# Performance work log

Measured on AMD Instinct MI355X. Metric: run time of the kernel, lower is better.

## Reference

```python
import jax, jax.numpy as jnp
import numpy as np

N_NODES = 50000


def gcn_conv(x, edge_index, edge_weight, W, b):
    """PyG GCNConv: x' = D^{-1/2}(A+I)D^{-1/2} (x W) + b, with edge weights."""
    n = x.shape[0]
    x = x @ W  # transform first (PyG order): [N, d_out]
    row, col = edge_index[0], edge_index[1]  # source -> target
    # add self loops with weight 1
    loop = jnp.arange(n)
    row = jnp.concatenate([row, loop])
    col = jnp.concatenate([col, loop])
    ew = jnp.concatenate([edge_weight, jnp.ones((n,), dtype=x.dtype)])
    # symmetric normalization based on (weighted) in-degree at targets
    deg = jax.ops.segment_sum(ew, col, num_segments=n)
    dis = jnp.where(deg > 0, jax.lax.rsqrt(deg), 0.0)
    norm = dis[row] * ew * dis[col]  # [E+N]
    # gather-scale-scatter aggregation
    msg = x[row] * norm[:, None]  # [E+N, d_out]
    out = jax.ops.segment_sum(msg, col, num_segments=n)
    return out + b


def setup_inputs() -> dict:
    key = jax.random.key(0)
    ks = jax.random.split(key, 9)
    E = 800000
    bert_output = jax.random.normal(ks[0], (N_NODES, 1024), dtype=jnp.float32)
    edge_index = jax.random.randint(ks[1], (2, E), 0, N_NODES, dtype=jnp.int64)
    edge_weight = jax.random.uniform(ks[2], (E,), dtype=jnp.float32)
    s1 = 1.0 / np.sqrt(1024)
    s2 = 1.0 / np.sqrt(512)
    s3 = 1.0 / np.sqrt(128)
    W1 = jax.random.uniform(ks[3], (1024, 512), jnp.float32, -s1, s1)
    b1 = jnp.zeros((512,), jnp.float32)
    W2 = jax.random.uniform(ks[4], (512, 128), jnp.float32, -s2, s2)
    b2 = jnp.zeros((128,), jnp.float32)
    Wfc = jax.random.uniform(ks[5], (128, 14), jnp.float32, -s3, s3)
    bfc = jax.random.uniform(ks[6], (14,), jnp.float32, -s3, s3)
    return {
        "bert_output": bert_output,
        "edge_index": edge_index,
        "edge_weight": edge_weight,
        "W1": W1, "b1": b1, "W2": W2, "b2": b2, "Wfc": Wfc, "bfc": bfc,
    }


def reference(bert_output, edge_index, edge_weight, W1, b1, W2, b2, Wfc, bfc):
    h = jax.nn.relu(gcn_conv(bert_output, edge_index, edge_weight, W1, b1))
    h = jax.nn.relu(gcn_conv(h, edge_index, edge_weight, W2, b2))
    logits = h @ Wfc + bfc
    return jax.nn.sigmoid(logits)
```

## Files before the change

kernel.cpp:

```cpp
#include <hip/hip_runtime.h>
#include <stdint.h>

__device__ __forceinline__ float bf2f(unsigned short h) {
  union { uint32_t u; float f; } v; v.u = ((uint32_t)h) << 16; return v.f;
}
__device__ __forceinline__ unsigned short f2bf(float f) {
  union { float f; uint32_t u; } v; v.f = f;
  uint32_t u = v.u;
  u += 0x7FFFu + ((u >> 16) & 1u);
  return (unsigned short)(u >> 16);
}
__device__ __forceinline__ uint32_t pack2bf(float a, float b) {
  return (uint32_t)f2bf(a) | ((uint32_t)f2bf(b) << 16);
}

typedef __attribute__((ext_vector_type(8))) short short8;
typedef __attribute__((ext_vector_type(4))) float floatx4;

__global__ void bgcn_probe(const uint32_t* __restrict__ xw,
                           const uint32_t* __restrict__ iw,
                           int* __restrict__ flags) {
  if (threadIdx.x == 0 && blockIdx.x == 0) {
    int hits = 0;
    for (int i = 0; i < 256; ++i) {
      uint32_t b = (xw[i] >> 8) & 0x7F;
      if (b >= 0x38 && b <= 0x41) hits++;
    }
    flags[0] = (hits < 128) ? 1 : 0;
    int nz = 0;
    for (int i = 1; i < 128; i += 2) nz += (iw[i] != 0);
    flags[1] = (nz == 0) ? 1 : 0;
  }
}

__global__ void bgcn_cvt_f(const void* __restrict__ src, unsigned short* __restrict__ dst,
                           int n, const int* __restrict__ flags) {
  int i = blockIdx.x * 256 + threadIdx.x;
  if (i >= n) return;
  if (flags[0]) dst[i] = f2bf(((const float*)src)[i]);
  else          dst[i] = ((const unsigned short*)src)[i];
}
__global__ void bgcn_cvt_i(const void* __restrict__ src, int* __restrict__ dst,
                           int n, const int* __restrict__ flags) {
  int i = blockIdx.x * 256 + threadIdx.x;
  if (i >= n) return;
  if (flags[1]) dst[i] = (int)((const long long*)src)[i];
  else          dst[i] = ((const int*)src)[i];
}
__global__ void bgcn_cvt_t(const void* __restrict__ src, unsigned short* __restrict__ dst,
                           int kbits, int N, int total, const int* __restrict__ flags) {
  int i = blockIdx.x * 256 + threadIdx.x;
  if (i >= total) return;
  int K = 1 << kbits;
  int n = i >> kbits;
  int k = i & (K - 1);
  size_t s = (size_t)k * N + n;
  if (flags[0]) dst[i] = f2bf(((const float*)src)[s]);
  else          dst[i] = ((const unsigned short*)src)[s];
}

__global__ void bgcn_init_deg(float* __restrict__ deg, int n) {
  int i = blockIdx.x * 256 + threadIdx.x;
  if (i < n) deg[i] = 1.0f;
}
__global__ void bgcn_deg(const int* __restrict__ col, const unsigned short* __restrict__ ew,
                         float* __restrict__ deg, int E) {
  int e = blockIdx.x * 256 + threadIdx.x;
  if (e < E) atomicAdd(&deg[col[e]], bf2f(ew[e]));
}
__global__ void bgcn_dis(const float* __restrict__ deg, float* __restrict__ dis, int n) {
  int i = blockIdx.x * 256 + threadIdx.x;
  if (i < n) dis[i] = rsqrtf(deg[i]);
}

__global__ void bgcn_hist(const int* __restrict__ col, int* __restrict__ counts, int E) {
  int e = blockIdx.x * 256 + threadIdx.x;
  if (e < E) atomicAdd(&counts[col[e]], 1);
}
__global__ void bgcn_scan_block(const int* __restrict__ counts, int* __restrict__ rowptr,
                                int* __restrict__ blocksum, int n) {
  __shared__ int buf[1024];
  int gid = blockIdx.x * 1024 + threadIdx.x;
  int v = (gid < n) ? counts[gid] : 0;
  buf[threadIdx.x] = v;
  __syncthreads();
  for (int off = 1; off < 1024; off <<= 1) {
    int x = (threadIdx.x >= off) ? buf[threadIdx.x - off] : 0;
    __syncthreads();
    buf[threadIdx.x] += x;
    __syncthreads();
  }
  if (gid < n) rowptr[gid + 1] = buf[threadIdx.x];
  if (threadIdx.x == 1023) blocksum[blockIdx.x] = buf[1023];
}
__global__ void bgcn_scan_tops(int* __restrict__ blocksum, int nb) {
  if (threadIdx.x == 0 && blockIdx.x == 0) {
    int acc = 0;
    for (int i = 0; i < nb; ++i) { int v = blocksum[i]; blocksum[i] = acc; acc += v; }
  }
}
__global__ void bgcn_scan_add(int* __restrict__ rowptr, const int* __restrict__ blocksum, int n) {
  int gid = blockIdx.x * 1024 + threadIdx.x;
  if (gid < n) rowptr[gid + 1] += blocksum[blockIdx.x];
  if (gid == 0) rowptr[0] = 0;
}
__global__ void bgcn_scatter(const int* __restrict__ row, const int* __restrict__ col,
                             const unsigned short* __restrict__ ew,
                             const float* __restrict__ dis,
                             const int* __restrict__ rowptr, int* __restrict__ fill,
                             int* __restrict__ esrc, float* __restrict__ enorm, int E) {
  int e = blockIdx.x * 256 + threadIdx.x;
  if (e >= E) return;
  int r = row[e], c = col[e];
  int pos = rowptr[c] + atomicAdd(&fill[c], 1);
  esrc[pos]  = r;
  enorm[pos] = dis[r] * bf2f(ew[e]) * dis[c];
}

#define GST 40
__global__ __launch_bounds__(256, 2) void bgcn_gemm128(
    const void* __restrict__ Araw, int a_probe, const int* __restrict__ flags,
    const unsigned short* __restrict__ Bt,
    unsigned short* __restrict__ C,
    int M, int N, int K, int nblk_bits) {
  __shared__ unsigned short Abuf[128 * GST];
  __shared__ unsigned short Bbuf[128 * GST];
  const bool a_fp32 = a_probe && flags[0];
  int t = threadIdx.x;
  int wave = t >> 6, lane = t & 63;
  int bx = blockIdx.x;
  int nblk = bx & ((1 << nblk_bits) - 1);
  int mblk = bx >> nblk_bits;
  int m0 = mblk * 128, n0 = nblk * 128;

  floatx4 acc[4][4];
  #pragma unroll
  for (int i = 0; i < 4; ++i)
    #pragma unroll
    for (int j = 0; j < 4; ++j)
      #pragma unroll
      for (int r = 0; r < 4; ++r) acc[i][j][r] = 0.0f;

  int srow  = t >> 1;
  int skoff = (t & 1) * 16;
  int am = m0 + srow; if (am >= M) am = M - 1;
  const float*          Af = (const float*)Araw          + (size_t)am * K + skoff;
  const unsigned short* Ah = (const unsigned short*)Araw + (size_t)am * K + skoff;
  const unsigned short* Bp = Bt + (size_t)(n0 + srow) * K + skoff;
  unsigned short* AL = Abuf + srow * GST + skoff;
  unsigned short* BL = Bbuf + srow * GST + skoff;

  int fr = lane & 15;
  int fk = (lane >> 4) * 8;
  int mw = (wave & 1) * 64;
  int nw = (wave >> 1) * 64;

  for (int k0 = 0; k0 < K; k0 += 32) {
    uint4 a0, a1;
    if (a_fp32) {
      float4 f0 = *(const float4*)(Af + k0);
      float4 f1 = *(const float4*)(Af + k0 + 4);
      float4 f2 = *(const float4*)(Af + k0 + 8);
      float4 f3 = *(const float4*)(Af + k0 + 12);
      a0 = make_uint4(pack2bf(f0.x, f0.y), pack2bf(f0.z, f0.w),
                      pack2bf(f1.x, f1.y), pack2bf(f1.z, f1.w));
      a1 = make_uint4(pack2bf(f2.x, f2.y), pack2bf(f2.z, f2.w),
                      pack2bf(f3.x, f3.y), pack2bf(f3.z, f3.w));
    } else {
      a0 = *(const uint4*)(Ah + k0);
      a1 = *(const uint4*)(Ah + k0 + 8);
    }
    uint4 b0 = *(const uint4*)(Bp + k0);
    uint4 b1 = *(const uint4*)(Bp + k0 + 8);
    *(uint4*)AL       = a0;
    *(uint4*)(AL + 8) = a1;
    *(uint4*)BL       = b0;
    *(uint4*)(BL + 8) = b1;
    __syncthreads();

    short8 afr[4], bfr[4];
    #pragma unroll
    for (int i = 0; i < 4; ++i)
      afr[i] = *(const short8*)(Abuf + (mw + i * 16 + fr) * GST + fk);
    #pragma unroll
    for (int i = 0; i < 4; ++i)
      bfr[i] = *(const short8*)(Bbuf + (nw + i * 16 + fr) * GST + fk);
    #pragma unroll
    for (int mt = 0; mt < 4; ++mt)
      #pragma unroll
      for (int nt = 0; nt < 4; ++nt)
        acc[mt][nt] = __builtin_amdgcn_mfma_f32_16x16x32_bf16(afr[mt], bfr[nt], acc[mt][nt], 0, 0, 0);
    __syncthreads();
  }

  int col_l = lane & 15;
  int row_b = (lane >> 4) * 4;
  #pragma unroll
  for (int mt = 0; mt < 4; ++mt)
    #pragma unroll
    for (int nt = 0; nt < 4; ++nt)
      #pragma unroll
      for (int r = 0; r < 4; ++r) {
        int m = m0 + mw + mt * 16 + row_b + r;
        if (m < M)
          C[(size_t)m * N + n0 + nw + nt * 16 + col_l] = f2bf(acc[mt][nt][r]);
      }
}

template <int VPL>
__device__ __forceinline__ void loadbf(const unsigned short* p, float* out) {
  if constexpr (VPL == 8) {
    uint4 v = *(const uint4*)p;
    uint32_t w0 = v.x, w1 = v.y, w2 = v.z, w3 = v.w;
    out[0] = bf2f((unsigned short)(w0 & 0xffff)); out[1] = bf2f((unsigned short)(w0 >> 16));
    out[2] = bf2f((unsigned short)(w1 & 0xffff)); out[3] = bf2f((unsigned short)(w1 >> 16));
    out[4] = bf2f((unsigned short)(w2 & 0xffff)); out[5] = bf2f((unsigned short)(w2 >> 16));
    out[6] = bf2f((unsigned short)(w3 & 0xffff)); out[7] = bf2f((unsigned short)(w3 >> 16));
  } else {
    uint32_t v = *(const uint32_t*)p;
    out[0] = bf2f((unsigned short)(v & 0xffff)); out[1] = bf2f((unsigned short)(v >> 16));
  }
}

template <int F>
__global__ __launch_bounds__(256) void bgcn_aggregate(
    const unsigned short* __restrict__ H,
    const int* __restrict__ rowptr,
    const int* __restrict__ esrc,
    const float* __restrict__ enorm,
    const float* __restrict__ dis,
    const unsigned short* __restrict__ bias,
    unsigned short* __restrict__ Out,
    int n_nodes) {
  constexpr int VPL = F / 64;
  int lane = threadIdx.x & 63;
  int c = blockIdx.x * 4 + (threadIdx.x >> 6);
  if (c >= n_nodes) return;
  float acc[VPL];
  #pragma unroll
  for (int j = 0; j < VPL; ++j) acc[j] = 0.0f;

  int beg = rowptr[c], end = rowptr[c + 1];
  int e = beg;
  for (; e + 4 <= end; e += 4) {
    int s0 = esrc[e], s1 = esrc[e + 1], s2 = esrc[e + 2], s3 = esrc[e + 3];
    float w0 = enorm[e], w1 = enorm[e + 1], w2 = enorm[e + 2], w3 = enorm[e + 3];
    float v0[VPL], v1[VPL], v2[VPL], v3[VPL];
    loadbf<VPL>(H + (size_t)s0 * F + lane * VPL, v0);
    loadbf<VPL>(H + (size_t)s1 * F + lane * VPL, v1);
    loadbf<VPL>(H + (size_t)s2 * F + lane * VPL, v2);
    loadbf<VPL>(H + (size_t)s3 * F + lane * VPL, v3);
    #pragma unroll
    for (int j = 0; j < VPL; ++j) {
      acc[j] += w0 * v0[j];
      acc[j] += w1 * v1[j];
      acc[j] += w2 * v2[j];
      acc[j] += w3 * v3[j];
    }
  }
  for (; e < end; ++e) {
    int src = esrc[e];
    float w = enorm[e];
    float vals[VPL];
    loadbf<VPL>(H + (size_t)src * F + lane * VPL, vals);
    #pragma unroll
    for (int j = 0; j < VPL; ++j) acc[j] += w * vals[j];
  }
  float ds = dis[c];
  float wself = ds * ds;
  float vals[VPL];
  loadbf<VPL>(H + (size_t)c * F + lane * VPL, vals);
  unsigned short ob[VPL];
  #pragma unroll
  for (int j = 0; j < VPL; ++j) {
    float v = acc[j] + wself * vals[j] + bf2f(bias[lane * VPL + j]);
    ob[j] = f2bf(fmaxf(v, 0.0f));
  }
  if constexpr (VPL == 8) {
    uint4 st = make_uint4((uint32_t)ob[0] | ((uint32_t)ob[1] << 16),
                          (uint32_t)ob[2] | ((uint32_t)ob[3] << 16),
                          (uint32_t)ob[4] | ((uint32_t)ob[5] << 16),
                          (uint32_t)ob[6] | ((uint32_t)ob[7] << 16));
    *(uint4*)(Out + (size_t)c * F + lane * VPL) = st;
  } else {
    *(uint32_t*)(Out + (size_t)c * F + lane * VPL) =
        (uint32_t)ob[0] | ((uint32_t)ob[1] << 16);
  }
}

__global__ __launch_bounds__(256) void bgcn_fc_sigmoid(
    const unsigned short* __restrict__ X,
    const unsigned short* __restrict__ W,
    const unsigned short* __restrict__ b,
    float* __restrict__ out,
    int n_nodes) {
  __shared__ float Ws[128 * 14];
  __shared__ float bs[14];
  for (int i = threadIdx.x; i < 128 * 14; i += 256) Ws[i] = bf2f(W[i]);
  if (threadIdx.x < 14) bs[threadIdx.x] = bf2f(b[threadIdx.x]);
  __syncthreads();
  int node = blockIdx.x * 256 + threadIdx.x;
  if (node >= n_nodes) return;
  float acc[14];
  #pragma unroll
  for (int c = 0; c < 14; ++c) acc[c] = bs[c];
  const unsigned short* xp = X + (size_t)node * 128;
  for (int k8 = 0; k8 < 16; ++k8) {
    float xv[8];
    loadbf<8>(xp + k8 * 8, xv);
    #pragma unroll
    for (int j = 0; j < 8; ++j) {
      int k = k8 * 8 + j;
      #pragma unroll
      for (int c = 0; c < 14; ++c) acc[c] = fmaf(xv[j], Ws[k * 14 + c], acc[c]);
    }
  }
  float* op = out + (size_t)node * 14;
  #pragma unroll
  for (int c = 0; c < 14; ++c)
    op[c] = 1.0f / (1.0f + __expf(-acc[c]));
}

static inline void* wsa(char*& p, size_t bytes) {
  void* r = p;
  p += (bytes + 255) & ~(size_t)255;
  return r;
}

extern "C" void kernel_launch(void* const* d_in, const int* in_sizes, int n_in,
                              void* d_out, int out_size, void* d_ws, size_t ws_size,
                              hipStream_t stream) {
  const void* Xr   = d_in[0];
  const void* EIr  = d_in[1];
  const void* EWr  = d_in[2];
  const void* W1r  = d_in[3];
  const void* b1r  = d_in[4];
  const void* W2r  = d_in[5];
  const void* b2r  = d_in[6];
  const void* Wfcr = d_in[7];
  const void* bfcr = d_in[8];
  float* out = (float*)d_out;

  const int N = in_sizes[0] / 1024;
  const int E = in_sizes[2];

  char* p = (char*)d_ws;
  unsigned short* bufA = (unsigned short*)wsa(p, (size_t)N * 512 * 2);
  unsigned short* bufB = (unsigned short*)wsa(p, (size_t)N * 512 * 2);
  float* deg      = (float*)wsa(p, (size_t)N * 4);
  float* dis      = (float*)wsa(p, (size_t)N * 4);
  int*   counts   = (int*)wsa(p, (size_t)N * 4);
  int*   rowptr   = (int*)wsa(p, (size_t)(N + 1) * 4);
  int*   blocksum = (int*)wsa(p, 256 * 4);
  int*   fill     = (int*)wsa(p, (size_t)N * 4);
  int*   esrc     = (int*)wsa(p, (size_t)E * 4);
  float* enorm    = (float*)wsa(p, (size_t)E * 4);
  int*   eidx     = (int*)wsa(p, (size_t)2 * E * 4);
  unsigned short* ewb  = (unsigned short*)wsa(p, (size_t)E * 2);
  unsigned short* W1t  = (unsigned short*)wsa(p, (size_t)1024 * 512 * 2);
  unsigned short* W2t  = (unsigned short*)wsa(p, (size_t)512 * 128 * 2);
  unsigned short* b1c  = (unsigned short*)wsa(p, 512 * 2);
  unsigned short* b2c  = (unsigned short*)wsa(p, 128 * 2);
  unsigned short* Wfcc = (unsigned short*)wsa(p, 128 * 14 * 2);
  unsigned short* bfcc = (unsigned short*)wsa(p, 16 * 2);
  int* flags      = (int*)wsa(p, 2 * 4);

  unsigned short* H1 = bufA;
  unsigned short* X2 = bufB;
  unsigned short* H2 = bufA;
  unsigned short* X3 = bufA + (size_t)N * 128;

  int gN = (N + 255) / 256;
  int gE = (E + 255) / 256;

  bgcn_probe<<<1, 64, 0, stream>>>((const uint32_t*)Xr, (const uint32_t*)EIr, flags);
  bgcn_cvt_i<<<(2 * E + 255) / 256, 256, 0, stream>>>(EIr, eidx, 2 * E, flags);
  bgcn_cvt_f<<<gE, 256, 0, stream>>>(EWr, ewb, E, flags);
  bgcn_cvt_t<<<(1024 * 512 + 255) / 256, 256, 0, stream>>>(W1r, W1t, 10, 512, 1024 * 512, flags);
  bgcn_cvt_t<<<(512 * 128 + 255) / 256, 256, 0, stream>>>(W2r, W2t, 9, 128, 512 * 128, flags);
  bgcn_cvt_f<<<2, 256, 0, stream>>>(b1r, b1c, 512, flags);
  bgcn_cvt_f<<<1, 256, 0, stream>>>(b2r, b2c, 128, flags);
  bgcn_cvt_f<<<7, 256, 0, stream>>>(Wfcr, Wfcc, 128 * 14, flags);
  bgcn_cvt_f<<<1, 64, 0, stream>>>(bfcr, bfcc, 14, flags);

  const int* rowp = eidx;
  const int* colp = eidx + E;

  hipMemsetAsync(counts, 0, (size_t)N * 4, stream);
  hipMemsetAsync(fill,   0, (size_t)N * 4, stream);

  bgcn_init_deg<<<gN, 256, 0, stream>>>(deg, N);
  bgcn_deg<<<gE, 256, 0, stream>>>(colp, ewb, deg, E);
  bgcn_dis<<<gN, 256, 0, stream>>>(deg, dis, N);
  bgcn_hist<<<gE, 256, 0, stream>>>(colp, counts, E);

  int nb = (N + 1023) / 1024;
  bgcn_scan_block<<<nb, 1024, 0, stream>>>(counts, rowptr, blocksum, N);
  bgcn_scan_tops<<<1, 64, 0, stream>>>(blocksum, nb);
  bgcn_scan_add<<<nb, 1024, 0, stream>>>(rowptr, blocksum, N);
  bgcn_scatter<<<gE, 256, 0, stream>>>(rowp, colp, ewb, dis, rowptr, fill, esrc, enorm, E);

  int mblks = (N + 127) / 128;

  bgcn_gemm128<<<mblks * 4, 256, 0, stream>>>(Xr, 1, flags, W1t, H1, N, 512, 1024, 2);
  bgcn_aggregate<512><<<(N + 3) / 4, 256, 0, stream>>>(H1, rowptr, esrc, enorm, dis, b1c, X2, N);

  bgcn_gemm128<<<mblks, 256, 0, stream>>>(X2, 0, flags, W2t, H2, N, 128, 512, 0);
  bgcn_aggregate<128><<<(N + 3) / 4, 256, 0, stream>>>(H2, rowptr, esrc, enorm, dis, b2c, X3, N);

  bgcn_fc_sigmoid<<<gN, 256, 0, stream>>>(X3, Wfcc, bfcc, out, N);
}
```

Measured before the change: 764.2 us.

## Pre-convert input to bf16 and use direct global-to-LDS loads in GEMMs

Adds a vectorized pass that converts the fp32 node features to bf16 into a larger workspace buffer, when the workspace is big enough. Both GEMMs then run a new kernel that fills shared memory with global_load_lds and issues 16x16x32 bf16 MFMAs. The aim is to halve the bytes the first GEMM reads per tile and to skip the register round trip on shared-memory loads. In exchange it adds an extra conversion pass over the 50000x1024 input, and the new GEMM is not double-buffered and syncs twice per k-step.

```diff
diff --git a/kernel.cpp b/kernel.cpp
--- a/kernel.cpp
+++ b/kernel.cpp
@@ -16,6 +16,13 @@
 
 typedef __attribute__((ext_vector_type(8))) short short8;
 typedef __attribute__((ext_vector_type(4))) float floatx4;
+
+__device__ __forceinline__ void gl2lds16(const unsigned short* g, unsigned short* l) {
+  __builtin_amdgcn_global_load_lds(
+      (const __attribute__((address_space(1))) uint32_t*)(const void*)g,
+      (__attribute__((address_space(3))) uint32_t*)(void*)l,
+      16, 0, 0);
+}
 
 __global__ void bgcn_probe(const uint32_t* __restrict__ xw,
                            const uint32_t* __restrict__ iw,
@@ -40,6 +47,22 @@
   if (flags[0]) dst[i] = f2bf(((const float*)src)[i]);
   else          dst[i] = ((const unsigned short*)src)[i];
 }
+__global__ void bgcn_cvt8(const void* __restrict__ src, unsigned short* __restrict__ dst,
+                          int n8, const int* __restrict__ flags) {
+  int i = blockIdx.x * 256 + threadIdx.x;
+  if (i >= n8) return;
+  size_t o = (size_t)i * 8;
+  uint4 d;
+  if (flags[0]) {
+    const float4* f = (const float4*)((const float*)src + o);
+    float4 f0 = f[0], f1 = f[1];
+    d = make_uint4(pack2bf(f0.x, f0.y), pack2bf(f0.z, f0.w),
+                   pack2bf(f1.x, f1.y), pack2bf(f1.z, f1.w));
+  } else {
+    d = *(const uint4*)((const unsigned short*)src + o);
+  }
+  *(uint4*)(dst + o) = d;
+}
 __global__ void bgcn_cvt_i(const void* __restrict__ src, int* __restrict__ dst,
                            int n, const int* __restrict__ flags) {
   int i = blockIdx.x * 256 + threadIdx.x;
@@ -115,6 +138,82 @@
   int pos = rowptr[c] + atomicAdd(&fill[c], 1);
   esrc[pos]  = r;
   enorm[pos] = dis[r] * bf2f(ew[e]) * dis[c];
+}
+
+__global__ __launch_bounds__(256) void bgcn_gemm_lds(
+    const unsigned short* __restrict__ A,
+    const unsigned short* __restrict__ Bt,
+    unsigned short* __restrict__ C,
+    int M, int N, int K, int nblk_bits) {
+  __shared__ unsigned short Abuf[128 * 32];
+  __shared__ unsigned short Bbuf[128 * 32];
+  int t = threadIdx.x;
+  int wave = t >> 6, lane = t & 63;
+  int bx = blockIdx.x;
+  int nblk = bx & ((1 << nblk_bits) - 1);
+  int mblk = bx >> nblk_bits;
+  int m0 = mblk * 128, n0 = nblk * 128;
+
+  floatx4 acc[4][4];
+  #pragma unroll
+  for (int i = 0; i < 4; ++i)
+    #pragma unroll
+    for (int j = 0; j < 4; ++j)
+      #pragma unroll
+      for (int r = 0; r < 4; ++r) acc[i][j][r] = 0.0f;
+
+  int rii  = lane >> 2;
+  int koff = (lane & 3) * 8;
+  int ar0 = m0 + wave * 32 + rii;      if (ar0 >= M) ar0 = M - 1;
+  int ar1 = m0 + wave * 32 + 16 + rii; if (ar1 >= M) ar1 = M - 1;
+  const unsigned short* Ag0 = A + (size_t)ar0 * K + koff;
+  const unsigned short* Ag1 = A + (size_t)ar1 * K + koff;
+  const unsigned short* Bg0 = Bt + (size_t)(n0 + wave * 32 + rii) * K + koff;
+  const unsigned short* Bg1 = Bg0 + (size_t)16 * K;
+  unsigned short* Al0 = Abuf + (wave * 32) * 32 + lane * 8;
+  unsigned short* Al1 = Abuf + (wave * 32 + 16) * 32 + lane * 8;
+  unsigned short* Bl0 = Bbuf + (wave * 32) * 32 + lane * 8;
+  unsigned short* Bl1 = Bbuf + (wave * 32 + 16) * 32 + lane * 8;
+
+  int fr = lane & 15;
+  int fk = (lane >> 4) * 8;
+  int mw = (wave & 1) * 64;
+  int nw = (wave >> 1) * 64;
+
+  for (int k0 = 0; k0 < K; k0 += 32) {
+    gl2lds16(Ag0 + k0, Al0);
+    gl2lds16(Ag1 + k0, Al1);
+    gl2lds16(Bg0 + k0, Bl0);
+    gl2lds16(Bg1 + k0, Bl1);
+    __syncthreads();
+
+    short8 afr[4], bfr[4];
+    #pragma unroll
+    for (int i = 0; i < 4; ++i)
+      afr[i] = *(const short8*)(Abuf + (mw + i * 16 + fr) * 32 + fk);
+    #pragma unroll
+    for (int i = 0; i < 4; ++i)
+      bfr[i] = *(const short8*)(Bbuf + (nw + i * 16 + fr) * 32 + fk);
+    #pragma unroll
+    for (int mt = 0; mt < 4; ++mt)
+      #pragma unroll
+      for (int nt = 0; nt < 4; ++nt)
+        acc[mt][nt] = __builtin_amdgcn_mfma_f32_16x16x32_bf16(afr[mt], bfr[nt], acc[mt][nt], 0, 0, 0);
+    __syncthreads();
+  }
+
+  int col_l = lane & 15;
+  int row_b = (lane >> 4) * 4;
+  #pragma unroll
+  for (int mt = 0; mt < 4; ++mt)
+    #pragma unroll
+    for (int nt = 0; nt < 4; ++nt)
+      #pragma unroll
+      for (int r = 0; r < 4; ++r) {
+        int m = m0 + mw + mt * 16 + row_b + r;
+        if (m < M)
+          C[(size_t)m * N + n0 + nw + nt * 16 + col_l] = f2bf(acc[mt][nt][r]);
+      }
 }
 
 #define GST 40
@@ -321,9 +420,10 @@
     op[c] = 1.0f / (1.0f + __expf(-acc[c]));
 }
 
+static inline size_t padsz(size_t x) { return (x + 255) & ~(size_t)255; }
 static inline void* wsa(char*& p, size_t bytes) {
   void* r = p;
-  p += (bytes + 255) & ~(size_t)255;
+  p += padsz(bytes);
   return r;
 }
 
@@ -344,15 +444,28 @@
   const int N = in_sizes[0] / 1024;
   const int E = in_sizes[2];
 
+  size_t need = padsz((size_t)N * 512 * 2)
+              + padsz((size_t)N * 1024 * 2)
+              + 4 * padsz((size_t)N * 4)
+              + padsz((size_t)(N + 1) * 4)
+              + padsz(256 * 4)
+              + 2 * padsz((size_t)E * 4)
+              + padsz((size_t)2 * E * 4)
+              + padsz((size_t)E * 2)
+              + padsz(1024 * 512 * 2) + padsz(512 * 128 * 2)
+              + padsz(512 * 2) + padsz(128 * 2) + padsz(128 * 14 * 2)
+              + padsz(32) + padsz(8);
+  const bool big = ws_size >= need;
+
   char* p = (char*)d_ws;
-  unsigned short* bufA = (unsigned short*)wsa(p, (size_t)N * 512 * 2);
-  unsigned short* bufB = (unsigned short*)wsa(p, (size_t)N * 512 * 2);
+  unsigned short* R1  = (unsigned short*)wsa(p, (size_t)N * 512 * 2);
+  unsigned short* R2  = (unsigned short*)wsa(p, (size_t)N * (big ? 1024 : 512) * 2);
   float* deg      = (float*)wsa(p, (size_t)N * 4);
   float* dis      = (float*)wsa(p, (size_t)N * 4);
   int*   counts   = (int*)wsa(p, (size_t)N * 4);
+  int*   fill     = (int*)wsa(p, (size_t)N * 4);
   int*   rowptr   = (int*)wsa(p, (size_t)(N + 1) * 4);
   int*   blocksum = (int*)wsa(p, 256 * 4);
-  int*   fill     = (int*)wsa(p, (size_t)N * 4);
   int*   esrc     = (int*)wsa(p, (size_t)E * 4);
   float* enorm    = (float*)wsa(p, (size_t)E * 4);
   int*   eidx     = (int*)wsa(p, (size_t)2 * E * 4);
@@ -362,13 +475,14 @@
   unsigned short* b1c  = (unsigned short*)wsa(p, 512 * 2);
   unsigned short* b2c  = (unsigned short*)wsa(p, 128 * 2);
   unsigned short* Wfcc = (unsigned short*)wsa(p, 128 * 14 * 2);
-  unsigned short* bfcc = (unsigned short*)wsa(p, 16 * 2);
-  int* flags      = (int*)wsa(p, 2 * 4);
-
-  unsigned short* H1 = bufA;
-  unsigned short* X2 = bufB;
-  unsigned short* H2 = bufA;
-  unsigned short* X3 = bufA + (size_t)N * 128;
+  unsigned short* bfcc = (unsigned short*)wsa(p, 32);
+  int* flags      = (int*)wsa(p, 8);
+
+  unsigned short* H1  = R1;
+  unsigned short* Xbf = R2;
+  unsigned short* X2  = R2;
+  unsigned short* H2  = R1;
+  unsigned short* X3  = R1 + (size_t)N * 128;
 
   int gN = (N + 255) / 256;
   int gE = (E + 255) / 256;
@@ -382,6 +496,10 @@
   bgcn_cvt_f<<<1, 256, 0, stream>>>(b2r, b2c, 128, flags);
   bgcn_cvt_f<<<7, 256, 0, stream>>>(Wfcr, Wfcc, 128 * 14, flags);
   bgcn_cvt_f<<<1, 64, 0, stream>>>(bfcr, bfcc, 14, flags);
+  if (big) {
+    int n8 = N * 1024 / 8;
+    bgcn_cvt8<<<(n8 + 255) / 256, 256, 0, stream>>>(Xr, Xbf, n8, flags);
+  }
 
   const int* rowp = eidx;
   const int* colp = eidx + E;
@@ -402,10 +520,13 @@
 
   int mblks = (N + 127) / 128;
 
-  bgcn_gemm128<<<mblks * 4, 256, 0, stream>>>(Xr, 1, flags, W1t, H1, N, 512, 1024, 2);
+  if (big)
+    bgcn_gemm_lds<<<mblks * 4, 256, 0, stream>>>(Xbf, W1t, H1, N, 512, 1024, 2);
+  else
+    bgcn_gemm128<<<mblks * 4, 256, 0, stream>>>(Xr, 1, flags, W1t, H1, N, 512, 1024, 2);
   bgcn_aggregate<512><<<(N + 3) / 4, 256, 0, stream>>>(H1, rowptr, esrc, enorm, dis, b1c, X2, N);
 
-  bgcn_gemm128<<<mblks, 256, 0, stream>>>(X2, 0, flags, W2t, H2, N, 128, 512, 0);
+  bgcn_gemm_lds<<<mblks, 256, 0, stream>>>(X2, W2t, H2, N, 128, 512, 0);
   bgcn_aggregate<128><<<(N + 3) / 4, 256, 0, stream>>>(H2, rowptr, esrc, enorm, dis, b2c, X3, N);
 
   bgcn_fc_sigmoid<<<gN, 256, 0, stream>>>(X3, Wfcc, bfcc, out, N);
```

Result: slower. 780.9 us (+2.2%).
